# Performance work log

Measured on AMD Instinct MI355X. Metric: run time of the kernel, lower is better.

Reference implementation:

```python
import jax, jax.numpy as jnp
import numpy as np

B, C_IN, C_OUT, H, W, W_DIM, K = 4, 64, 64, 512, 512, 512, 3
LRELU_SLOPE = 0.2
ACT_GAIN = np.sqrt(2.0).astype(np.float32)  # lrelu def_gain
CONV_CLAMP = 256.0


def setup_inputs() -> dict:
    key = jax.random.key(0)
    ks = jax.random.split(key, 5)
    return {
        "x": jax.random.normal(ks[0], (B, C_IN, H, W), dtype=jnp.float32),
        "ws": jax.random.normal(ks[1], (B, W_DIM), dtype=jnp.float32),
        "noise": jax.random.normal(ks[2], (B, 1, H, W), dtype=jnp.float32),
        "affine_weight": jax.random.normal(ks[3], (C_IN, W_DIM), dtype=jnp.float32),
        "affine_bias": jnp.ones((C_IN,), dtype=jnp.float32),
        "conv_weight": jax.random.normal(ks[4], (C_OUT, C_IN, K, K), dtype=jnp.float32),
        "bias": jnp.zeros((C_OUT,), dtype=jnp.float32),
    }


def reference(x, ws, noise, affine_weight, affine_bias, conv_weight, bias):
    b, c_in, h, w_sp = x.shape
    c_out, _, kh, kw = conv_weight.shape
    w_dim = ws.shape[1]

    # Affine (FullyConnectedLayer with equalized LR: weight_gain = 1/sqrt(w_dim), bias_init=1)
    styles = ws @ (affine_weight.T * np.float32(1.0 / np.sqrt(w_dim))) + affine_bias  # [b, c_in]

    # Modulate per-sample weights: w = weight[None] * styles
    wmod = conv_weight[None] * styles[:, None, :, None, None]  # [b, c_out, c_in, kh, kw]

    # Demodulation coefficients
    demod = jax.lax.rsqrt(jnp.sum(jnp.square(wmod), axis=(2, 3, 4)) + 1e-8)  # [b, c_out]
    wmod = wmod * demod[:, :, None, None, None]

    # Fused grouped conv: groups = batch (conv2d_resample, up=down=1, flip_weight=True -> correlation)
    xg = x.reshape(1, b * c_in, h, w_sp)
    wg = wmod.reshape(b * c_out, c_in, kh, kw)
    pad = kh // 2
    y = jax.lax.conv_general_dilated(
        xg, wg, window_strides=(1, 1), padding=[(pad, pad), (pad, pad)],
        dimension_numbers=("NCHW", "OIHW", "NCHW"), feature_group_count=b)
    y = y.reshape(b, c_out, h, w_sp)

    # Noise add (broadcast over channels)
    y = y + noise

    # bias_act: bias + lrelu * act_gain, then clamp (conv_clamp * gain, gain=1)
    y = y + bias[None, :, None, None]
    y = jnp.where(y >= 0, y, LRELU_SLOPE * y) * ACT_GAIN
    y = jnp.clip(y, -CONV_CLAMP, CONV_CLAMP)
    return y
```

## Files before the change

kernel.cpp:

```cpp
#include <hip/hip_runtime.h>
#include <math.h>

#define HH 512
#define WW 512
#define HW (HH * WW)
#define PW 514
#define PPIX (PW * PW)

#define A_U 36864
#define B_U 22016
#define LDS_BYTES ((A_U + 2 * B_U) * 2)

typedef short bf16x8 __attribute__((ext_vector_type(8)));
typedef float f32x4  __attribute__((ext_vector_type(4)));
typedef float f32x16 __attribute__((ext_vector_type(16)));

__device__ __forceinline__ ushort f2bf(float f) {
    union { float f; uint u; } c; c.f = f;
    uint u = c.u;
    return (ushort)((u + 0x7fffu + ((u >> 16) & 1u)) >> 16);
}

__device__ __forceinline__ uint cvtpk(float a, float b) {
    uint r;
    asm("v_cvt_pk_bf16_f32 %0, %1, %2" : "=v"(r) : "v"(a), "v"(b));
    return r;
}

__global__ void k_styles(const float* __restrict__ wsv, const float* __restrict__ aw,
                         const float* __restrict__ ab, float* __restrict__ styles) {
    int bid = blockIdx.x;
    int b = bid >> 6, ci = bid & 63;
    int l = threadIdx.x;
    const float* wrow = wsv + b * 512;
    const float* arow = aw + ci * 512;
    float s = 0.f;
    #pragma unroll
    for (int j = 0; j < 8; ++j)
        s += wrow[l + 64 * j] * arow[l + 64 * j];
    #pragma unroll
    for (int off = 32; off; off >>= 1)
        s += __shfl_xor(s, off, 64);
    if (l == 0)
        styles[b * 64 + ci] = s * 0.044194173824159216f + ab[ci];
}

__global__ void k_wmod(const float* __restrict__ cw, const float* __restrict__ styles,
                       ushort* __restrict__ wb) {
    int b = blockIdx.x >> 6, co = blockIdx.x & 63;
    int ci = threadIdx.x;
    float st = styles[b * 64 + ci];
    const float* wp = cw + (co * 64 + ci) * 9;
    float wv[9];
    float ss = 0.f;
    #pragma unroll
    for (int k = 0; k < 9; ++k) { wv[k] = wp[k] * st; ss += wv[k] * wv[k]; }
    #pragma unroll
    for (int off = 32; off; off >>= 1)
        ss += __shfl_xor(ss, off, 64);
    float dm = 1.0f / sqrtf(ss + 1e-8f);
    int cisw = ((((ci >> 3) ^ co) & 7) << 3) | (ci & 7);
    #pragma unroll
    for (int k = 0; k < 9; ++k)
        wb[((size_t)(b * 64 + co) * 9 + k) * 64 + cisw] = f2bf(wv[k] * dm);
}

__global__ __launch_bounds__(256) void k_xpose(
    const float* __restrict__ x, ushort* __restrict__ xp) {
    const int t = threadIdx.x;
    const int bid = blockIdx.x;

    if (bid >= 8192) {
        int id = (bid - 8192) * 256 + t;
        if (id >= 4 * 2052) return;
        int b = id / 2052, r = id % 2052;
        int gyp, gxp;
        if (r < 514)       { gyp = 0;        gxp = r; }
        else if (r < 1028) { gyp = 513;      gxp = r - 514; }
        else if (r < 1540) { gyp = r - 1027; gxp = 0; }
        else               { gyp = r - 1539; gxp = 513; }
        ushort* p = xp + (((size_t)b * PW + gyp) * PW + gxp) * 64;
        uint4 z = make_uint4(0, 0, 0, 0);
        #pragma unroll
        for (int i = 0; i < 8; ++i) *(uint4*)(p + i * 8) = z;
        return;
    }

    __shared__ ushort lt[128 * 68];
    const int gxt = bid & 3;
    const int gy  = (bid >> 2) & 511;
    const int b   = bid >> 11;

    const float* xb = x + (size_t)b * 64 * HW + (size_t)gy * WW + gxt * 128;
    const int ci0 = 8 * (t >> 5);
    const int gxc = t & 31;

    f32x4 v[8];
    #pragma unroll
    for (int j = 0; j < 8; ++j)
        v[j] = *(const f32x4*)(xb + (size_t)(ci0 + j) * HW + gxc * 4);

    #pragma unroll
    for (int p = 0; p < 4; ++p) {
        int px = gxc * 4 + p;
        int rowp = ((px & 3) * 32 + (px >> 2)) * 68;
        #pragma unroll
        for (int cg = 0; cg < 2; ++cg) {
            uint lo = cvtpk(v[4 * cg + 0][p], v[4 * cg + 1][p]);
            uint hi = cvtpk(v[4 * cg + 2][p], v[4 * cg + 3][p]);
            *(uint2*)&lt[rowp + ci0 + 4 * cg] = make_uint2(lo, hi);
        }
    }
    __syncthreads();

    const int px = t >> 1, half = t & 1;
    const int rowp = ((px & 3) * 32 + (px >> 2)) * 68 + half * 32;
    uint4 o0 = *(uint4*)&lt[rowp + 0];
    uint4 o1 = *(uint4*)&lt[rowp + 8];
    uint4 o2 = *(uint4*)&lt[rowp + 16];
    uint4 o3 = *(uint4*)&lt[rowp + 24];
    ushort* dst = xp + (((size_t)b * PW + (gy + 1)) * PW + (gxt * 128 + px + 1)) * 64
                     + half * 32;
    *(uint4*)(dst + 0)  = o0;
    *(uint4*)(dst + 8)  = o1;
    *(uint4*)(dst + 16) = o2;
    *(uint4*)(dst + 24) = o3;
}

__global__ __launch_bounds__(512, 1) void k_conv(
    const ushort* __restrict__ xp,
    const ushort* __restrict__ wb,
    const float* __restrict__ noise,
    const float* __restrict__ bias,
    float* __restrict__ out) {
    extern __shared__ __align__(16) ushort lds[];

    const int t = threadIdx.x;
    const int w = t >> 6;
    const int lane = t & 63;
    const int n5 = lane & 31;
    const int hl = lane >> 5;
    const int mtw = w >> 2;
    const int rp  = w & 3;
    const int blk = blockIdx.x;
    const int b = blk >> 6;
    const int band = blk & 63;
    const int ty = band * 8;

    const ushort* xpb = xp + (size_t)b * PPIX * 64;
    const ushort* wA  = wb + (size_t)b * 64 * 576;

    #pragma unroll
    for (int jj = 0; jj < 9; ++jj) {
        int j = w + jj * 8;
        const ushort* src = wA + j * 512 + lane * 8;
        __builtin_amdgcn_global_load_lds(
            (const __attribute__((address_space(1))) unsigned int*)src,
            (__attribute__((address_space(3))) unsigned int*)&lds[j * 512],
            16, 0, 0);
    }

    int soff[6];
    #pragma unroll
    for (int jj = 0; jj < 6; ++jj) {
        int j = w + jj * 8;
        if (j < 43) {
            int c = j * 64 + lane;
            int c2 = c < 2719 ? c : 2719;
            int cig = c2 & 7;
            int pxl = c2 >> 3;
            int row = pxl / 34;
            int lcol = pxl - row * 34;
            int gsrc = cig ^ (lcol & 7);
            soff[jj] = ((ty + row) * PW + lcol) * 64 + gsrc * 8;
        } else soff[jj] = 0;
    }

    #pragma unroll
    for (int jj = 0; jj < 6; ++jj) {
        int j = w + jj * 8;
        if (j < 43)
            __builtin_amdgcn_global_load_lds(
                (const __attribute__((address_space(1))) unsigned int*)(xpb + soff[jj]),
                (__attribute__((address_space(3))) unsigned int*)&lds[A_U + j * 512],
                16, 0, 0);
    }
    asm volatile("s_waitcnt vmcnt(0)" ::: "memory");
    __syncthreads();

    const int aidx = (mtw * 32 + n5) * 576 + ((hl ^ (n5 & 7)) << 3);

    int bidx[2][3];
    const int brow = 2 * rp + (n5 >> 4);
    #pragma unroll
    for (int i = 0; i < 2; ++i)
        #pragma unroll
        for (int dx = 0; dx < 3; ++dx) {
            int lcol = i * 16 + (n5 & 15) + dx;
            bidx[i][dx] = (brow * 34 + lcol) * 64 + ((hl ^ (lcol & 7)) << 3);
        }

    const float* nz = noise + (size_t)b * HW;
    const int orow = ty + brow;

    int p = 0;
    for (int it = 0; it < 16; ++it) {
        const int tx = it * 32;

        float nv[2];
        #pragma unroll
        for (int i = 0; i < 2; ++i)
            nv[i] = nz[orow * WW + tx + i * 16 + (n5 & 15)];

        if (it < 15) {
            #pragma unroll
            for (int jj = 0; jj < 6; ++jj) {
                int j = w + jj * 8;
                if (j < 43)
                    __builtin_amdgcn_global_load_lds(
                        (const __attribute__((address_space(1))) unsigned int*)
                            (xpb + soff[jj] + (tx + 32) * 64),
                        (__attribute__((address_space(3))) unsigned int*)
                            &lds[A_U + (p ^ 1) * B_U + j * 512],
                        16, 0, 0);
            }
        }

        const ushort* bufp = &lds[A_U + p * B_U];
        f32x16 acc[2];
        #pragma unroll
        for (int i = 0; i < 2; ++i)
            acc[i] = (f32x16){0.f,0.f,0.f,0.f,0.f,0.f,0.f,0.f,
                              0.f,0.f,0.f,0.f,0.f,0.f,0.f,0.f};

        #pragma unroll
        for (int dy = 0; dy < 3; ++dy) {
            #pragma unroll
            for (int dx = 0; dx < 3; ++dx) {
                const int off = dy * 3 + dx;
                #pragma unroll
                for (int kb = 0; kb < 4; ++kb) {
                    bf16x8 afr, bfr[2];
                    afr = *(const bf16x8*)&lds[(aidx + off * 64) ^ (kb << 4)];
                    #pragma unroll
                    for (int i = 0; i < 2; ++i)
                        bfr[i] = *(const bf16x8*)
                            &bufp[(bidx[i][dx] + dy * (34 * 64)) ^ (kb << 4)];
                    #pragma unroll
                    for (int i = 0; i < 2; ++i)
                        acc[i] = __builtin_amdgcn_mfma_f32_32x32x16_bf16(
                            afr, bfr[i], acc[i], 0, 0, 0);
                }
            }
        }

        #pragma unroll
        for (int i = 0; i < 2; ++i) {
            const int ocol = tx + i * 16 + (n5 & 15);
            #pragma unroll
            for (int reg = 0; reg < 16; ++reg) {
                int co = mtw * 32 + (reg & 3) + 8 * (reg >> 2) + 4 * hl;
                float y = acc[i][reg] + nv[i] + bias[co];
                y = (y >= 0.f ? y : 0.2f * y) * 1.41421356237f;
                y = fminf(fmaxf(y, -256.f), 256.f);
                out[((size_t)(b * 64 + co) * HH + orow) * WW + ocol] = y;
            }
        }

        asm volatile("s_waitcnt vmcnt(32)" ::: "memory");
        __builtin_amdgcn_sched_barrier(0);
        __builtin_amdgcn_s_barrier();
        p ^= 1;
    }
}

extern "C" void kernel_launch(void* const* d_in, const int* in_sizes, int n_in,
                              void* d_out, int out_size, void* d_ws, size_t ws_size,
                              hipStream_t stream) {
    const float* x     = (const float*)d_in[0];
    const float* wsv   = (const float*)d_in[1];
    const float* noise = (const float*)d_in[2];
    const float* aw    = (const float*)d_in[3];
    const float* ab    = (const float*)d_in[4];
    const float* cw    = (const float*)d_in[5];
    const float* bias  = (const float*)d_in[6];
    float* out = (float*)d_out;

    float*  styles = (float*)d_ws;
    ushort* wb16   = (ushort*)((char*)d_ws + 1024);
    ushort* xpad   = (ushort*)((char*)d_ws + (1 << 20));

    hipFuncSetAttribute((const void*)k_conv,
                        hipFuncAttributeMaxDynamicSharedMemorySize, LDS_BYTES);

    k_styles<<<256, 64, 0, stream>>>(wsv, aw, ab, styles);
    k_wmod<<<256, 64, 0, stream>>>(cw, styles, wb16);
    k_xpose<<<8225, 256, 0, stream>>>(x, xpad);
    k_conv<<<256, 512, LDS_BYTES, stream>>>(xpad, wb16, noise, bias, out);
}
```

Before: 234.7 us.

## Split conv by output-channel half and pipeline input-channel halves through LDS

Each conv block now covers 32 output channels with 256 threads (512 blocks), so LDS per block shrinks to 80KB and more blocks can reside per CU. The input tile is staged in two input-channel halves: one half is computed while the other is loaded. Stores of the previous tile are deferred so they overlap the next tile's compute. Band order is permuted for locality. The cost is that each input tile is loaded twice, once per channel half, and the loop has more barriers and waitcnt points.

Measured after the change: 242.2 us. 3.2% more time.

```diff
diff --git a/kernel.cpp b/kernel.cpp
--- a/kernel.cpp
+++ b/kernel.cpp
@@ -7,9 +7,11 @@
 #define PW 514
 #define PPIX (PW * PW)
 
-#define A_U 36864
-#define B_U 22016
-#define LDS_BYTES ((A_U + 2 * B_U) * 2)
+#define A_U    18432
+#define B0_U   18432
+#define B1_U   29696
+#define B_ALLOC 11264
+#define LDS_BYTES 81920
 
 typedef short bf16x8 __attribute__((ext_vector_type(8)));
 typedef float f32x4  __attribute__((ext_vector_type(4)));
@@ -127,7 +129,7 @@
     *(uint4*)(dst + 24) = o3;
 }
 
-__global__ __launch_bounds__(512, 1) void k_conv(
+__global__ __launch_bounds__(256) void k_conv(
     const ushort* __restrict__ xp,
     const ushort* __restrict__ wb,
     const float* __restrict__ noise,
@@ -140,19 +142,19 @@
     const int lane = t & 63;
     const int n5 = lane & 31;
     const int hl = lane >> 5;
-    const int mtw = w >> 2;
-    const int rp  = w & 3;
     const int blk = blockIdx.x;
-    const int b = blk >> 6;
-    const int band = blk & 63;
+    const int b   = blk >> 7;
+    const int coh = (blk >> 6) & 1;
+    const int j64 = blk & 63;
+    const int band = (j64 & 7) * 8 + (j64 >> 3);
     const int ty = band * 8;
 
     const ushort* xpb = xp + (size_t)b * PPIX * 64;
-    const ushort* wA  = wb + (size_t)b * 64 * 576;
+    const ushort* wA  = wb + (size_t)(b * 64 + coh * 32) * 576;
 
     #pragma unroll
     for (int jj = 0; jj < 9; ++jj) {
-        int j = w + jj * 8;
+        int j = w + jj * 4;
         const ushort* src = wA + j * 512 + lane * 8;
         __builtin_amdgcn_global_load_lds(
             (const __attribute__((address_space(1))) unsigned int*)src,
@@ -163,47 +165,55 @@
     int soff[6];
     #pragma unroll
     for (int jj = 0; jj < 6; ++jj) {
-        int j = w + jj * 8;
-        if (j < 43) {
-            int c = j * 64 + lane;
-            int c2 = c < 2719 ? c : 2719;
-            int cig = c2 & 7;
-            int pxl = c2 >> 3;
+        int j = w + jj * 4;
+        if (j < 22) {
+            int u = j * 512 + lane * 8;
+            int u2 = u < 10872 ? u : 10872;
+            int pxl = u2 >> 5;
+            int cig = (u2 >> 3) & 3;
             int row = pxl / 34;
             int lcol = pxl - row * 34;
-            int gsrc = cig ^ (lcol & 7);
+            int gsrc = cig ^ (lcol & 3);
             soff[jj] = ((ty + row) * PW + lcol) * 64 + gsrc * 8;
         } else soff[jj] = 0;
     }
 
-    #pragma unroll
-    for (int jj = 0; jj < 6; ++jj) {
-        int j = w + jj * 8;
-        if (j < 43)
-            __builtin_amdgcn_global_load_lds(
-                (const __attribute__((address_space(1))) unsigned int*)(xpb + soff[jj]),
-                (__attribute__((address_space(3))) unsigned int*)&lds[A_U + j * 512],
-                16, 0, 0);
-    }
+    auto stage_b = [&](int bufu, int txn, int h) {
+        #pragma unroll
+        for (int jj = 0; jj < 6; ++jj) {
+            int j = w + jj * 4;
+            if (j < 22)
+                __builtin_amdgcn_global_load_lds(
+                    (const __attribute__((address_space(1))) unsigned int*)
+                        (xpb + soff[jj] + txn * 64 + h * 32),
+                    (__attribute__((address_space(3))) unsigned int*)
+                        &lds[bufu + j * 512],
+                    16, 0, 0);
+        }
+    };
+
+    stage_b(B0_U, 0, 0);
     asm volatile("s_waitcnt vmcnt(0)" ::: "memory");
     __syncthreads();
 
-    const int aidx = (mtw * 32 + n5) * 576 + ((hl ^ (n5 & 7)) << 3);
+    const int aidx = n5 * 576 + ((hl ^ (n5 & 7)) << 3);
 
     int bidx[2][3];
-    const int brow = 2 * rp + (n5 >> 4);
+    const int brow = 2 * w + (n5 >> 4);
     #pragma unroll
     for (int i = 0; i < 2; ++i)
         #pragma unroll
         for (int dx = 0; dx < 3; ++dx) {
             int lcol = i * 16 + (n5 & 15) + dx;
-            bidx[i][dx] = (brow * 34 + lcol) * 64 + ((hl ^ (lcol & 7)) << 3);
+            bidx[i][dx] = (brow * 34 + lcol) * 32 + ((hl ^ (lcol & 3)) << 3);
         }
 
     const float* nz = noise + (size_t)b * HW;
     const int orow = ty + brow;
-
-    int p = 0;
+    const size_t outb = (size_t)(b * 64 + coh * 32) * HW;
+
+    f32x16 acc[2];
+
     for (int it = 0; it < 16; ++it) {
         const int tx = it * 32;
 
@@ -212,65 +222,100 @@
         for (int i = 0; i < 2; ++i)
             nv[i] = nz[orow * WW + tx + i * 16 + (n5 & 15)];
 
-        if (it < 15) {
-            #pragma unroll
-            for (int jj = 0; jj < 6; ++jj) {
-                int j = w + jj * 8;
-                if (j < 43)
-                    __builtin_amdgcn_global_load_lds(
-                        (const __attribute__((address_space(1))) unsigned int*)
-                            (xpb + soff[jj] + (tx + 32) * 64),
-                        (__attribute__((address_space(3))) unsigned int*)
-                            &lds[A_U + (p ^ 1) * B_U + j * 512],
-                        16, 0, 0);
-            }
-        }
-
-        const ushort* bufp = &lds[A_U + p * B_U];
-        f32x16 acc[2];
+        stage_b(B1_U, tx, 1);
+
+        if (it > 0) {
+            const int ptx = tx - 32;
+            #pragma unroll
+            for (int i = 0; i < 2; ++i) {
+                const int ocol = ptx + i * 16 + (n5 & 15);
+                #pragma unroll
+                for (int reg = 0; reg < 16; ++reg) {
+                    int co = (reg & 3) + 8 * (reg >> 2) + 4 * hl;
+                    out[outb + (size_t)co * HW + (size_t)orow * WW + ocol] = acc[i][reg];
+                }
+            }
+        }
+
         #pragma unroll
         for (int i = 0; i < 2; ++i)
             acc[i] = (f32x16){0.f,0.f,0.f,0.f,0.f,0.f,0.f,0.f,
                               0.f,0.f,0.f,0.f,0.f,0.f,0.f,0.f};
-
         #pragma unroll
         for (int dy = 0; dy < 3; ++dy) {
             #pragma unroll
             for (int dx = 0; dx < 3; ++dx) {
                 const int off = dy * 3 + dx;
                 #pragma unroll
-                for (int kb = 0; kb < 4; ++kb) {
-                    bf16x8 afr, bfr[2];
-                    afr = *(const bf16x8*)&lds[(aidx + off * 64) ^ (kb << 4)];
+                for (int kb = 0; kb < 2; ++kb) {
+                    bf16x8 afr = *(const bf16x8*)
+                        &lds[(aidx + off * 64) ^ (kb << 4)];
                     #pragma unroll
-                    for (int i = 0; i < 2; ++i)
-                        bfr[i] = *(const bf16x8*)
-                            &bufp[(bidx[i][dx] + dy * (34 * 64)) ^ (kb << 4)];
+                    for (int i = 0; i < 2; ++i) {
+                        bf16x8 bfr = *(const bf16x8*)
+                            &lds[B0_U + ((bidx[i][dx] + dy * (34 * 32)) ^ (kb << 4))];
+                        acc[i] = __builtin_amdgcn_mfma_f32_32x32x16_bf16(
+                            afr, bfr, acc[i], 0, 0, 0);
+                    }
+                }
+            }
+        }
+
+        if (it == 0) { asm volatile("s_waitcnt vmcnt(0)" ::: "memory"); }
+        else         { asm volatile("s_waitcnt vmcnt(32)" ::: "memory"); }
+        __builtin_amdgcn_sched_barrier(0);
+        __builtin_amdgcn_s_barrier();
+
+        if (it < 15) stage_b(B0_U, tx + 32, 0);
+
+        #pragma unroll
+        for (int dy = 0; dy < 3; ++dy) {
+            #pragma unroll
+            for (int dx = 0; dx < 3; ++dx) {
+                const int off = dy * 3 + dx;
+                #pragma unroll
+                for (int kb = 0; kb < 2; ++kb) {
+                    bf16x8 afr = *(const bf16x8*)
+                        &lds[(aidx + off * 64) ^ ((2 + kb) << 4)];
                     #pragma unroll
-                    for (int i = 0; i < 2; ++i)
+                    for (int i = 0; i < 2; ++i) {
+                        bf16x8 bfr = *(const bf16x8*)
+                            &lds[B1_U + ((bidx[i][dx] + dy * (34 * 32)) ^ (kb << 4))];
                         acc[i] = __builtin_amdgcn_mfma_f32_32x32x16_bf16(
-                            afr, bfr[i], acc[i], 0, 0, 0);
+                            afr, bfr, acc[i], 0, 0, 0);
+                    }
                 }
             }
         }
 
         #pragma unroll
         for (int i = 0; i < 2; ++i) {
-            const int ocol = tx + i * 16 + (n5 & 15);
             #pragma unroll
             for (int reg = 0; reg < 16; ++reg) {
-                int co = mtw * 32 + (reg & 3) + 8 * (reg >> 2) + 4 * hl;
-                float y = acc[i][reg] + nv[i] + bias[co];
+                int co = (reg & 3) + 8 * (reg >> 2) + 4 * hl;
+                float y = acc[i][reg] + nv[i] + bias[coh * 32 + co];
                 y = (y >= 0.f ? y : 0.2f * y) * 1.41421356237f;
                 y = fminf(fmaxf(y, -256.f), 256.f);
-                out[((size_t)(b * 64 + co) * HH + orow) * WW + ocol] = y;
-            }
-        }
-
-        asm volatile("s_waitcnt vmcnt(32)" ::: "memory");
+                acc[i][reg] = y;
+            }
+        }
+
+        asm volatile("s_waitcnt vmcnt(0)" ::: "memory");
         __builtin_amdgcn_sched_barrier(0);
         __builtin_amdgcn_s_barrier();
-        p ^= 1;
+    }
+
+    {
+        const int ptx = 15 * 32;
+        #pragma unroll
+        for (int i = 0; i < 2; ++i) {
+            const int ocol = ptx + i * 16 + (n5 & 15);
+            #pragma unroll
+            for (int reg = 0; reg < 16; ++reg) {
+                int co = (reg & 3) + 8 * (reg >> 2) + 4 * hl;
+                out[outb + (size_t)co * HW + (size_t)orow * WW + ocol] = acc[i][reg];
+            }
+        }
     }
 }
 
@@ -296,5 +341,5 @@
     k_styles<<<256, 64, 0, stream>>>(wsv, aw, ab, styles);
     k_wmod<<<256, 64, 0, stream>>>(cw, styles, wb16);
     k_xpose<<<8225, 256, 0, stream>>>(x, xpad);
-    k_conv<<<256, 512, LDS_BYTES, stream>>>(xpad, wb16, noise, bias, out);
-}
+    k_conv<<<512, 256, LDS_BYTES, stream>>>(xpad, wb16, noise, bias, out);
+}
```
